# Kernel tuning notes

Hardware: AMD Instinct MI355X
Metric: run time of the kernel (lower is better)

The kernel has to match this reference:

```python
import jax, jax.numpy as jnp
import numpy as np

STRIDE = (1, 1)
PADDING = ((1, 1), (1, 1))


def setup_inputs() -> dict:
    key = jax.random.key(0)
    kx, kw, kb = jax.random.split(key, 3)
    x = jax.random.normal(kx, (32, 128, 56, 56), dtype=jnp.float32)
    weight = jax.random.normal(kw, (256, 128, 3, 3), dtype=jnp.float32)  # (O, I, kh, kw)
    bias = jax.random.normal(kb, (256,), dtype=jnp.float32)
    return {"x": x, "weight": weight, "bias": bias}


def reference(x, weight, bias):
    # Faithful dense 2D convolution (cross-correlation, as in the torch module),
    # NCHW input, OIHW weight, stride 1, padding 1.
    out = jax.lax.conv_general_dilated(
        x, weight,
        window_strides=STRIDE,
        padding=PADDING,
        dimension_numbers=("NCHW", "OIHW", "NCHW"),
    )
    return out + bias[None, :, None, None]
```

## Files before the change

### kernel.cpp

```cpp
#include <hip/hip_runtime.h>

#define C_IN   128
#define H_IN   56
#define W_IN   56
#define HW     3136
#define CHW    401408
#define O_OUT  256
#define OHW    802816

#define BM 256
#define BN 128
#define LDSW 64
#define LDK 72
#define XTP 132

typedef __bf16 bf16x8 __attribute__((ext_vector_type(8)));
typedef float  f32x4  __attribute__((ext_vector_type(4)));
typedef unsigned short ushort_t;
typedef ushort_t ushort8 __attribute__((ext_vector_type(8)));

__device__ __forceinline__ ushort_t f2bf(float f) {
    union { float f; unsigned u; } v; v.f = f;
    unsigned r = (v.u + 0x7fffu + ((v.u >> 16) & 1u)) >> 16;
    return (ushort_t)r;
}

__global__ void wt_kernel(const float* __restrict__ w, ushort_t* __restrict__ wbf) {
    int idx = blockIdx.x * 256 + threadIdx.x;
    if (idx >= 9 * 256 * 128) return;
    int pos = idx >> 15;
    int rem = idx & 32767;
    int o   = rem >> 7;
    int c   = rem & 127;
    wbf[idx] = f2bf(w[o * 1152 + c * 9 + pos]);
}

__global__ __launch_bounds__(256)
void xt_kernel(const float* __restrict__ x, ushort_t* __restrict__ xb) {
    __shared__ ushort_t T[64 * XTP];
    const int t  = threadIdx.x;
    const int tb = blockIdx.x;
    const int n   = tb / 49;
    const int hw0 = (tb - n * 49) * 64;
    const float* src = x + (long)n * CHW + hw0;

    #pragma unroll
    for (int i = 0; i < 8; ++i) {
        const int g  = i * 256 + t;
        const int c  = g >> 4;
        const int p4 = g & 15;
        f32x4 v = *(const f32x4*)(src + (long)c * HW + p4 * 4);
        #pragma unroll
        for (int j = 0; j < 4; ++j)
            T[(p4 * 4 + j) * XTP + c] = f2bf(v[j]);
    }
    __syncthreads();

    ushort_t* dst = xb + ((long)n * HW + hw0) * 128;
    #pragma unroll
    for (int s = 0; s < 4; ++s) {
        const int idx = s * 256 + t;
        const int pix = idx >> 4;
        const int grp = idx & 15;
        ushort8 v = *(const ushort8*)(&T[pix * XTP + grp * 8]);
        *(ushort8*)(dst + pix * 128 + grp * 8) = v;
    }
}

__global__ __launch_bounds__(512, 4)
void conv2_kernel(const ushort_t* __restrict__ xb, const ushort_t* __restrict__ wbf,
                  const float* __restrict__ bias, float* __restrict__ out) {
    __shared__ ushort_t As[BM * LDSW];
    __shared__ ushort_t Bs[BN * LDSW];

    const int tid  = threadIdx.x;
    const int lane = tid & 63;
    const int wave = tid >> 6;
    const int wm   = wave >> 1;
    const int wn   = wave & 1;
    const int l15  = lane & 15;
    const int quad = lane >> 4;

    const int pix_base = blockIdx.x * BN;

    const int bpx = tid >> 2;
    const int bg0 = (tid & 3) * 2;
    const int p   = pix_base + bpx;
    const int n_img = p / HW;
    const int hw    = p - n_img * HW;
    const int h     = hw / W_IN;
    const int w_    = hw - h * W_IN;

    const int ao = tid >> 3;
    const int ag = tid & 7;

    f32x4 acc[4][4];
    #pragma unroll
    for (int t = 0; t < 4; ++t)
        #pragma unroll
        for (int u = 0; u < 4; ++u)
            acc[t][u] = f32x4{0.f, 0.f, 0.f, 0.f};

    for (int pos = 0; pos < 9; ++pos) {
        const int dh = pos / 3 - 1;
        const int dw = pos - (pos / 3) * 3 - 1;
        const int ih = h + dh;
        const int iw = w_ + dw;
        const bool valid = ((unsigned)ih < (unsigned)H_IN) && ((unsigned)iw < (unsigned)W_IN);
        const ushort_t* bsrc = xb + (long)(p + dh * W_IN + dw) * 128;

        #pragma unroll
        for (int half = 0; half < 2; ++half) {
            const int c0 = half * 64;

            {
                const ushort_t* wsrc = wbf + pos * 32768 + c0;
                #pragma unroll
                for (int s = 0; s < 4; ++s) {
                    const int o = ao + s * 64;
                    ushort8 v = *(const ushort8*)(wsrc + (o << 7) + ag * 8);
                    *(ushort8*)(&As[o * LDSW + ((ag ^ (o & 7)) * 8)]) = v;
                }
            }
            {
                #pragma unroll
                for (int q = 0; q < 2; ++q) {
                    const int g = bg0 + q;
                    ushort8 v;
                    if (valid) v = *(const ushort8*)(bsrc + c0 + g * 8);
                    else       v = ushort8{0,0,0,0,0,0,0,0};
                    *(ushort8*)(&Bs[bpx * LDSW + ((g ^ (bpx & 7)) * 8)]) = v;
                }
            }
            __syncthreads();

            #pragma unroll
            for (int ks = 0; ks < 2; ++ks) {
                bf16x8 af[4], bfv[4];
                const int k16 = ks * 4 + quad;
                #pragma unroll
                for (int t = 0; t < 4; ++t) {
                    const int row = wm * 64 + t * 16 + l15;
                    af[t] = *(const bf16x8*)(&As[row * LDSW + ((k16 ^ (row & 7)) * 8)]);
                }
                #pragma unroll
                for (int u = 0; u < 4; ++u) {
                    const int col = wn * 64 + u * 16 + l15;
                    bfv[u] = *(const bf16x8*)(&Bs[col * LDSW + ((k16 ^ (col & 7)) * 8)]);
                }
                #pragma unroll
                for (int t = 0; t < 4; ++t)
                    #pragma unroll
                    for (int u = 0; u < 4; ++u)
                        acc[t][u] = __builtin_amdgcn_mfma_f32_16x16x32_bf16(af[t], bfv[u], acc[t][u], 0, 0, 0);
            }
            __syncthreads();
        }
    }

    #pragma unroll
    for (int u = 0; u < 4; ++u) {
        const int col = wn * 64 + u * 16 + l15;
        const int pp  = pix_base + col;
        const int nn  = pp / HW;
        const int hw2 = pp - nn * HW;
        const long obase = (long)nn * OHW + hw2;
        #pragma unroll
        for (int t = 0; t < 4; ++t) {
            const int o_base = wm * 64 + t * 16 + quad * 4;
            #pragma unroll
            for (int r = 0; r < 4; ++r) {
                const int o = o_base + r;
                out[obase + (long)o * HW] = acc[t][u][r] + bias[o];
            }
        }
    }
}

__global__ __launch_bounds__(512, 4)
void conv_kernel(const float* __restrict__ x, const ushort_t* __restrict__ wbf,
                 const float* __restrict__ bias, float* __restrict__ out) {
    __shared__ ushort_t As[BM * LDK];
    __shared__ ushort_t Bs[BN * LDK];

    const int tid  = threadIdx.x;
    const int lane = tid & 63;
    const int wave = tid >> 6;
    const int wm   = wave >> 1;
    const int wn   = wave & 1;
    const int l15  = lane & 15;
    const int quad = lane >> 4;

    const int pix_base = blockIdx.x * BN;
    const int px  = tid & 127;
    const int cg0 = tid >> 7;
    const int p   = pix_base + px;
    const int n_img = p / HW;
    const int hw    = p - n_img * HW;
    const int h     = hw / W_IN;
    const int w_    = hw - h * W_IN;
    const float* ximg = x + (long)n_img * CHW;

    f32x4 acc[4][4];
    #pragma unroll
    for (int t = 0; t < 4; ++t)
        #pragma unroll
        for (int u = 0; u < 4; ++u)
            acc[t][u] = f32x4{0.f, 0.f, 0.f, 0.f};

    for (int pos = 0; pos < 9; ++pos) {
        const int dh = pos / 3 - 1;
        const int dw = pos - (pos / 3) * 3 - 1;
        const int ih = h + dh;
        const int iw = w_ + dw;
        const bool valid = ((unsigned)ih < (unsigned)H_IN) && ((unsigned)iw < (unsigned)W_IN);
        const float* xsrc = ximg + ih * W_IN + iw;

        for (int half = 0; half < 2; ++half) {
            const int c0 = half * 64;
            {
                const ushort_t* wsrc = wbf + ((pos * 256) << 7) + c0;
                #pragma unroll
                for (int s = 0; s < 4; ++s) {
                    const int o  = (tid >> 3) + s * 64;
                    const int cg = tid & 7;
                    ushort8 v = *(const ushort8*)(wsrc + (o << 7) + cg * 8);
                    *(ushort8*)(&As[o * LDK + cg * 8]) = v;
                }
            }
            {
                #pragma unroll
                for (int s = 0; s < 2; ++s) {
                    const int cg = cg0 + s * 4;
                    const float* src = xsrc + (long)(c0 + cg * 8) * HW;
                    ushort8 v;
                    #pragma unroll
                    for (int j = 0; j < 8; ++j) {
                        float f = valid ? src[j * HW] : 0.0f;
                        v[j] = f2bf(f);
                    }
                    *(ushort8*)(&Bs[px * LDK + cg * 8]) = v;
                }
            }
            __syncthreads();

            #pragma unroll
            for (int ks = 0; ks < 2; ++ks) {
                bf16x8 af[4], bfv[4];
                #pragma unroll
                for (int t = 0; t < 4; ++t) {
                    const int row = wm * 64 + t * 16 + l15;
                    af[t] = *(const bf16x8*)(&As[row * LDK + ks * 32 + quad * 8]);
                }
                #pragma unroll
                for (int u = 0; u < 4; ++u) {
                    const int col = wn * 64 + u * 16 + l15;
                    bfv[u] = *(const bf16x8*)(&Bs[col * LDK + ks * 32 + quad * 8]);
                }
                #pragma unroll
                for (int t = 0; t < 4; ++t)
                    #pragma unroll
                    for (int u = 0; u < 4; ++u)
                        acc[t][u] = __builtin_amdgcn_mfma_f32_16x16x32_bf16(af[t], bfv[u], acc[t][u], 0, 0, 0);
            }
            __syncthreads();
        }
    }

    #pragma unroll
    for (int u = 0; u < 4; ++u) {
        const int col = wn * 64 + u * 16 + l15;
        const int pp  = pix_base + col;
        const int hw2 = pp - (pp / HW) * HW;
        const long obase = (long)(pp / HW) * OHW + hw2;
        #pragma unroll
        for (int t = 0; t < 4; ++t) {
            const int o_base = wm * 64 + t * 16 + quad * 4;
            #pragma unroll
            for (int r = 0; r < 4; ++r) {
                const int o = o_base + r;
                out[obase + (long)o * HW] = acc[t][u][r] + bias[o];
            }
        }
    }
}

extern "C" void kernel_launch(void* const* d_in, const int* in_sizes, int n_in,
                              void* d_out, int out_size, void* d_ws, size_t ws_size,
                              hipStream_t stream) {
    const float* x    = (const float*)d_in[0];
    const float* w    = (const float*)d_in[1];
    const float* bias = (const float*)d_in[2];
    float* out        = (float*)d_out;

    ushort_t* wbf = (ushort_t*)d_ws;
    ushort_t* xb  = (ushort_t*)((char*)d_ws + 589824);

    const size_t need = 589824u + 25690112u;

    hipLaunchKernelGGL(wt_kernel, dim3(1152), dim3(256), 0, stream, w, wbf);
    if (ws_size >= need) {
        hipLaunchKernelGGL(xt_kernel, dim3(1568), dim3(256), 0, stream, x, xb);
        hipLaunchKernelGGL(conv2_kernel, dim3(100352 / BN), dim3(512), 0, stream,
                           xb, wbf, bias, out);
    } else {
        hipLaunchKernelGGL(conv_kernel, dim3(100352 / BN), dim3(512), 0, stream,
                           x, wbf, bias, out);
    }
}
```

Baseline: 226.2 us.

## Pad activations, double-buffer async LDS loads, read weights directly from global

Stores the bf16 NHWC activations into a zero-padded 58x58 buffer, with a new kernel that zeroes the border, so the conv kernel no longer needs bounds checks per tap. The new conv kernel stages each tap's full 128-channel pixel tile into LDS with global_load_lds, double-buffered so the next tap's load overlaps the current MFMAs, and it syncs once per tap instead of twice per half. Weights are no longer staged in LDS. MFMA A fragments are read straight from global or cache, which frees LDS and halves the barriers but adds global-load latency inside the inner loop. The transpose kernel now packs channel pairs into 32-bit words and uses a 65-word padded row to avoid LDS bank conflicts.

After: 328.1 us. 45.0% more time.

```diff
diff --git a/kernel.cpp b/kernel.cpp
--- a/kernel.cpp
+++ b/kernel.cpp
@@ -7,22 +7,28 @@
 #define CHW    401408
 #define O_OUT  256
 #define OHW    802816
-
-#define BM 256
-#define BN 128
-#define LDSW 64
-#define LDK 72
-#define XTP 132
+#define HP     58
+#define WP     58
+#define HWP    3364
+#define BN     128
+#define LDK    72
 
 typedef __bf16 bf16x8 __attribute__((ext_vector_type(8)));
 typedef float  f32x4  __attribute__((ext_vector_type(4)));
 typedef unsigned short ushort_t;
 typedef ushort_t ushort8 __attribute__((ext_vector_type(8)));
+typedef unsigned int u32;
 
 __device__ __forceinline__ ushort_t f2bf(float f) {
     union { float f; unsigned u; } v; v.f = f;
     unsigned r = (v.u + 0x7fffu + ((v.u >> 16) & 1u)) >> 16;
     return (ushort_t)r;
+}
+
+__device__ __forceinline__ void gload_lds16(const ushort_t* g, ushort_t* l) {
+    __builtin_amdgcn_global_load_lds(
+        (const __attribute__((address_space(1))) u32*)g,
+        (__attribute__((address_space(3))) u32*)l, 16, 0, 0);
 }
 
 __global__ void wt_kernel(const float* __restrict__ w, ushort_t* __restrict__ wbf) {
@@ -35,9 +41,23 @@
     wbf[idx] = f2bf(w[o * 1152 + c * 9 + pos]);
 }
 
+__global__ void bz_kernel(ushort_t* __restrict__ xbp) {
+    int idx = blockIdx.x * 256 + threadIdx.x;
+    if (idx >= 32 * 228 * 16) return;
+    int grp = idx & 15;
+    int bp  = (idx >> 4) % 228;
+    int n   = (idx >> 4) / 228;
+    int h_p, w_p;
+    if (bp < 58)       { h_p = 0;  w_p = bp; }
+    else if (bp < 116) { h_p = 57; w_p = bp - 58; }
+    else { int r = bp - 116; h_p = 1 + (r >> 1); w_p = (r & 1) ? 57 : 0; }
+    ushort8 z = ushort8{0,0,0,0,0,0,0,0};
+    *(ushort8*)(xbp + ((long)n * HWP + h_p * WP + w_p) * 128 + grp * 8) = z;
+}
+
 __global__ __launch_bounds__(256)
-void xt_kernel(const float* __restrict__ x, ushort_t* __restrict__ xb) {
-    __shared__ ushort_t T[64 * XTP];
+void xt_kernel(const float* __restrict__ x, ushort_t* __restrict__ xbp) {
+    __shared__ u32 T[64 * 65];
     const int t  = threadIdx.x;
     const int tb = blockIdx.x;
     const int n   = tb / 49;
@@ -45,33 +65,40 @@
     const float* src = x + (long)n * CHW + hw0;
 
     #pragma unroll
-    for (int i = 0; i < 8; ++i) {
-        const int g  = i * 256 + t;
-        const int c  = g >> 4;
-        const int p4 = g & 15;
-        f32x4 v = *(const f32x4*)(src + (long)c * HW + p4 * 4);
-        #pragma unroll
-        for (int j = 0; j < 4; ++j)
-            T[(p4 * 4 + j) * XTP + c] = f2bf(v[j]);
+    for (int i = 0; i < 4; ++i) {
+        const int cpair = i * 16 + (t >> 4);
+        const int p4    = t & 15;
+        f32x4 a = *(const f32x4*)(src + (long)(2 * cpair) * HW + p4 * 4);
+        f32x4 b = *(const f32x4*)(src + (long)(2 * cpair + 1) * HW + p4 * 4);
+        #pragma unroll
+        for (int j = 0; j < 4; ++j) {
+            u32 pack = (u32)f2bf(a[j]) | ((u32)f2bf(b[j]) << 16);
+            T[(p4 * 4 + j) * 65 + cpair] = pack;
+        }
     }
     __syncthreads();
 
-    ushort_t* dst = xb + ((long)n * HW + hw0) * 128;
     #pragma unroll
     for (int s = 0; s < 4; ++s) {
         const int idx = s * 256 + t;
         const int pix = idx >> 4;
-        const int grp = idx & 15;
-        ushort8 v = *(const ushort8*)(&T[pix * XTP + grp * 8]);
-        *(ushort8*)(dst + pix * 128 + grp * 8) = v;
+        const int g   = idx & 15;
+        u32 d0 = T[pix * 65 + g * 4 + 0];
+        u32 d1 = T[pix * 65 + g * 4 + 1];
+        u32 d2 = T[pix * 65 + g * 4 + 2];
+        u32 d3 = T[pix * 65 + g * 4 + 3];
+        const int hw = hw0 + pix;
+        const int h  = hw / 56;
+        const int w  = hw - h * 56;
+        u32* dst = (u32*)(xbp + ((long)n * HWP + (h + 1) * WP + (w + 1)) * 128 + g * 8);
+        dst[0] = d0; dst[1] = d1; dst[2] = d2; dst[3] = d3;
     }
 }
 
 __global__ __launch_bounds__(512, 4)
-void conv2_kernel(const ushort_t* __restrict__ xb, const ushort_t* __restrict__ wbf,
+void conv3_kernel(const ushort_t* __restrict__ xbp, const ushort_t* __restrict__ wbf,
                   const float* __restrict__ bias, float* __restrict__ out) {
-    __shared__ ushort_t As[BM * LDSW];
-    __shared__ ushort_t Bs[BN * LDSW];
+    __shared__ ushort_t Bs[2][BN * 128];
 
     const int tid  = threadIdx.x;
     const int lane = tid & 63;
@@ -80,19 +107,22 @@
     const int wn   = wave & 1;
     const int l15  = lane & 15;
     const int quad = lane >> 4;
-
     const int pix_base = blockIdx.x * BN;
 
-    const int bpx = tid >> 2;
-    const int bg0 = (tid & 3) * 2;
-    const int p   = pix_base + bpx;
-    const int n_img = p / HW;
-    const int hw    = p - n_img * HW;
-    const int h     = hw / W_IN;
-    const int w_    = hw - h * W_IN;
-
-    const int ao = tid >> 3;
-    const int ag = tid & 7;
+    const int spx = tid >> 4;
+    const int gsw = tid & 15;
+    int sbase[4];
+    #pragma unroll
+    for (int r = 0; r < 4; ++r) {
+        const int pix = r * 32 + spx;
+        const int p   = pix_base + pix;
+        const int n   = p / HW;
+        const int hw  = p - n * HW;
+        const int h   = hw / W_IN;
+        const int w   = hw - h * W_IN;
+        const int g   = gsw ^ (pix & 15);
+        sbase[r] = (int)(((long)n * HWP + (h + 1) * WP + (w + 1)) * 128 + g * 8);
+    }
 
     f32x4 acc[4][4];
     #pragma unroll
@@ -101,61 +131,48 @@
         for (int u = 0; u < 4; ++u)
             acc[t][u] = f32x4{0.f, 0.f, 0.f, 0.f};
 
+    {
+        #pragma unroll
+        for (int r = 0; r < 4; ++r)
+            gload_lds16(xbp + sbase[r] + (-WP - 1) * 128, &Bs[0][(r * 512 + tid) * 8]);
+    }
+    __syncthreads();
+
+    #pragma unroll
     for (int pos = 0; pos < 9; ++pos) {
-        const int dh = pos / 3 - 1;
-        const int dw = pos - (pos / 3) * 3 - 1;
-        const int ih = h + dh;
-        const int iw = w_ + dw;
-        const bool valid = ((unsigned)ih < (unsigned)H_IN) && ((unsigned)iw < (unsigned)W_IN);
-        const ushort_t* bsrc = xb + (long)(p + dh * W_IN + dw) * 128;
-
-        #pragma unroll
-        for (int half = 0; half < 2; ++half) {
-            const int c0 = half * 64;
-
-            {
-                const ushort_t* wsrc = wbf + pos * 32768 + c0;
-                #pragma unroll
-                for (int s = 0; s < 4; ++s) {
-                    const int o = ao + s * 64;
-                    ushort8 v = *(const ushort8*)(wsrc + (o << 7) + ag * 8);
-                    *(ushort8*)(&As[o * LDSW + ((ag ^ (o & 7)) * 8)]) = v;
-                }
-            }
-            {
-                #pragma unroll
-                for (int q = 0; q < 2; ++q) {
-                    const int g = bg0 + q;
-                    ushort8 v;
-                    if (valid) v = *(const ushort8*)(bsrc + c0 + g * 8);
-                    else       v = ushort8{0,0,0,0,0,0,0,0};
-                    *(ushort8*)(&Bs[bpx * LDSW + ((g ^ (bpx & 7)) * 8)]) = v;
-                }
-            }
-            __syncthreads();
-
-            #pragma unroll
-            for (int ks = 0; ks < 2; ++ks) {
-                bf16x8 af[4], bfv[4];
-                const int k16 = ks * 4 + quad;
-                #pragma unroll
-                for (int t = 0; t < 4; ++t) {
-                    const int row = wm * 64 + t * 16 + l15;
-                    af[t] = *(const bf16x8*)(&As[row * LDSW + ((k16 ^ (row & 7)) * 8)]);
-                }
-                #pragma unroll
-                for (int u = 0; u < 4; ++u) {
-                    const int col = wn * 64 + u * 16 + l15;
-                    bfv[u] = *(const bf16x8*)(&Bs[col * LDSW + ((k16 ^ (col & 7)) * 8)]);
-                }
-                #pragma unroll
-                for (int t = 0; t < 4; ++t)
-                    #pragma unroll
-                    for (int u = 0; u < 4; ++u)
-                        acc[t][u] = __builtin_amdgcn_mfma_f32_16x16x32_bf16(af[t], bfv[u], acc[t][u], 0, 0, 0);
-            }
-            __syncthreads();
-        }
+        const int cur = pos & 1;
+        if (pos < 8) {
+            const int npos = pos + 1;
+            const int dh = npos / 3 - 1;
+            const int dw = npos - (npos / 3) * 3 - 1;
+            const int off = (dh * WP + dw) * 128;
+            #pragma unroll
+            for (int r = 0; r < 4; ++r)
+                gload_lds16(xbp + sbase[r] + off, &Bs[1 - cur][(r * 512 + tid) * 8]);
+        }
+        const ushort_t* wsrc = wbf + pos * 32768;
+
+        #pragma unroll
+        for (int ks = 0; ks < 4; ++ks) {
+            bf16x8 af[4], bfv[4];
+            #pragma unroll
+            for (int t = 0; t < 4; ++t) {
+                const int o = wm * 64 + t * 16 + l15;
+                af[t] = *(const bf16x8*)(wsrc + o * 128 + ks * 32 + quad * 8);
+            }
+            const int gk = ks * 4 + quad;
+            #pragma unroll
+            for (int u = 0; u < 4; ++u) {
+                const int col = wn * 64 + u * 16 + l15;
+                bfv[u] = *(const bf16x8*)(&Bs[cur][col * 128 + ((gk ^ (col & 15)) * 8)]);
+            }
+            #pragma unroll
+            for (int t = 0; t < 4; ++t)
+                #pragma unroll
+                for (int u = 0; u < 4; ++u)
+                    acc[t][u] = __builtin_amdgcn_mfma_f32_16x16x32_bf16(af[t], bfv[u], acc[t][u], 0, 0, 0);
+        }
+        __syncthreads();
     }
 
     #pragma unroll
@@ -180,7 +197,7 @@
 __global__ __launch_bounds__(512, 4)
 void conv_kernel(const float* __restrict__ x, const ushort_t* __restrict__ wbf,
                  const float* __restrict__ bias, float* __restrict__ out) {
-    __shared__ ushort_t As[BM * LDK];
+    __shared__ ushort_t As[256 * LDK];
     __shared__ ushort_t Bs[BN * LDK];
 
     const int tid  = threadIdx.x;
@@ -271,8 +288,9 @@
     for (int u = 0; u < 4; ++u) {
         const int col = wn * 64 + u * 16 + l15;
         const int pp  = pix_base + col;
-        const int hw2 = pp - (pp / HW) * HW;
-        const long obase = (long)(pp / HW) * OHW + hw2;
+        const int nn  = pp / HW;
+        const int hw2 = pp - nn * HW;
+        const long obase = (long)nn * OHW + hw2;
         #pragma unroll
         for (int t = 0; t < 4; ++t) {
             const int o_base = wm * 64 + t * 16 + quad * 4;
@@ -294,15 +312,16 @@
     float* out        = (float*)d_out;
 
     ushort_t* wbf = (ushort_t*)d_ws;
-    ushort_t* xb  = (ushort_t*)((char*)d_ws + 589824);
-
-    const size_t need = 589824u + 25690112u;
+    ushort_t* xbp = (ushort_t*)((char*)d_ws + 589824);
+
+    const size_t need = 589824u + 27557888u;
 
     hipLaunchKernelGGL(wt_kernel, dim3(1152), dim3(256), 0, stream, w, wbf);
     if (ws_size >= need) {
-        hipLaunchKernelGGL(xt_kernel, dim3(1568), dim3(256), 0, stream, x, xb);
-        hipLaunchKernelGGL(conv2_kernel, dim3(100352 / BN), dim3(512), 0, stream,
-                           xb, wbf, bias, out);
+        hipLaunchKernelGGL(bz_kernel, dim3(456), dim3(256), 0, stream, xbp);
+        hipLaunchKernelGGL(xt_kernel, dim3(1568), dim3(256), 0, stream, x, xbp);
+        hipLaunchKernelGGL(conv3_kernel, dim3(100352 / BN), dim3(512), 0, stream,
+                           xbp, wbf, bias, out);
     } else {
         hipLaunchKernelGGL(conv_kernel, dim3(100352 / BN), dim3(512), 0, stream,
                            x, wbf, bias, out);
```
